# Optimization experiments

Measured on AMD Instinct MI355X. Metric: run time of the kernel, lower is better.

## Reference

```python
import jax, jax.numpy as jnp
import numpy as np

N = 16384          # input points
F = 128            # feature dim (x is (N, 3+F))
POOL = 4           # pooling_factor
M = N // POOL      # number of FPS query points
K = 16             # num_neighbors


def setup_inputs() -> dict:
    key = jax.random.key(0)
    x = jax.random.normal(key, (N, 3 + F), dtype=jnp.float32)
    return {"x": x}


def _fps(coords, m):
    """Furthest point sampling: coords (N,3) -> m indices. Deterministic start at 0."""
    n = coords.shape[0]

    def step(carry, _):
        min_d2, last = carry
        d2 = jnp.sum((coords - coords[last]) ** 2, axis=-1)  # (N,)
        min_d2 = jnp.minimum(min_d2, d2)
        nxt = jnp.argmax(min_d2).astype(jnp.int32)
        return (min_d2, nxt), nxt

    init = (jnp.full((n,), jnp.inf, dtype=coords.dtype), jnp.int32(0))
    _, idxs = jax.lax.scan(step, init, None, length=m - 1)
    return jnp.concatenate([jnp.zeros((1,), dtype=jnp.int32), idxs])


def reference(x):
    coords = x[:, :3]                          # (N,3)
    fps_idx = _fps(coords, M)                  # (M,)
    q_points = coords[fps_idx]                 # (M,3)

    # knn neighbor query: squared distances (M,N), take K nearest
    d2 = jnp.sum((q_points[:, None, :] - coords[None, :, :]) ** 2, axis=-1)
    _, nbr_idx = jax.lax.top_k(-d2, K)         # (M,K)

    s_feats = x[nbr_idx, 3:]                   # (M,K,F) gather
    pooled = jnp.max(s_feats, axis=1)          # feat_mapping='max' -> (M,F)
    return jnp.concatenate([q_points, pooled], axis=-1)  # (M, 3+F)
```

## Files before the change

kernel.cpp:

```cpp
#include <hip/hip_runtime.h>

#define N_PTS 16384
#define ROWF  131
#define M_OUT 4096
#define KNN   16
#define FPS_T 1024

typedef unsigned long long u64;
typedef float f32x2 __attribute__((ext_vector_type(2)));

template <int CTRL, int ROW_MASK>
__device__ __forceinline__ u64 kmax_dpp(u64 k) {
  const int lo = (int)(unsigned)k, hi = (int)(unsigned)(k >> 32);
  const int nlo = __builtin_amdgcn_update_dpp(lo, lo, CTRL, ROW_MASK, 0xf, false);
  const int nhi = __builtin_amdgcn_update_dpp(hi, hi, CTRL, ROW_MASK, 0xf, false);
  const u64 nk = ((u64)(unsigned)nhi << 32) | (unsigned)nlo;
  return nk > k ? nk : k;
}

__global__ void prep_kernel(const float* __restrict__ x,
                            float4* __restrict__ coords4) {
  const int p = blockIdx.x * blockDim.x + threadIdx.x;
  if (p < N_PTS) {
    coords4[p] = make_float4(x[p * ROWF + 0], x[p * ROWF + 1],
                             x[p * ROWF + 2], 0.0f);
  }
}

#define REP16R(F) F(15) F(14) F(13) F(12) F(11) F(10) F(9) F(8) \
                  F(7) F(6) F(5) F(4) F(3) F(2) F(1) F(0)
#define REPP(F) F(0,0,1) F(1,2,3) F(2,4,5) F(3,6,7) \
                F(4,8,9) F(5,10,11) F(6,12,13) F(7,14,15)

__global__
__attribute__((amdgpu_flat_work_group_size(FPS_T, FPS_T)))
__attribute__((amdgpu_waves_per_eu(4, 4)))
void fps_kernel(const float4* __restrict__ coords4, float* __restrict__ out) {
#pragma clang fp contract(off)
  __shared__ u64 s_wkey[2][16];
  const int tid = threadIdx.x, lane = tid & 63, wid = tid >> 6;

#define FPS_DECL(t,a,b) f32x2 PX##t, PY##t, PZ##t; float md##a, md##b;
  REPP(FPS_DECL)
#undef FPS_DECL

#define FPS_INIT(t,a,b) {                                                  \
    const float4 va = coords4[(a << 10) + tid];                            \
    const float4 vb = coords4[(b << 10) + tid];                            \
    PX##t = (f32x2){va.x, vb.x};                                           \
    PY##t = (f32x2){va.y, vb.y};                                           \
    PZ##t = (f32x2){va.z, vb.z};                                           \
    md##a = __int_as_float(0x7f800000);                                    \
    md##b = __int_as_float(0x7f800000); }
  REPP(FPS_INIT)
#undef FPS_INIT

  const float4 q0 = coords4[0];
  float qx = q0.x, qy = q0.y, qz = q0.z;
  if (tid == 0) { out[0] = qx; out[1] = qy; out[2] = qz; }

  for (int s = 1; s < M_OUT; ++s) {
    const f32x2 QX = {qx, qx}, QY = {qy, qy}, QZ = {qz, qz};

#define FPS_UPD(t,a,b) {                                                   \
    const f32x2 dx = PX##t - QX;                                           \
    const f32x2 dy = PY##t - QY;                                           \
    const f32x2 dz = PZ##t - QZ;                                           \
    const f32x2 xx = dx * dx;                                              \
    const f32x2 yy = dy * dy;                                              \
    const f32x2 zz = dz * dz;                                              \
    const f32x2 ss = xx + yy;                                              \
    const f32x2 d2 = ss + zz;                                              \
    md##a = fminf(md##a, d2.x);                                            \
    md##b = fminf(md##b, d2.y); }
    REPP(FPS_UPD)
#undef FPS_UPD

    const float a0 = fmaxf(fmaxf(md0,  md1),  md2);
    const float a1 = fmaxf(fmaxf(md3,  md4),  md5);
    const float a2 = fmaxf(fmaxf(md6,  md7),  md8);
    const float a3 = fmaxf(fmaxf(md9,  md10), md11);
    const float a4 = fmaxf(fmaxf(md12, md13), md14);
    const float b0 = fmaxf(fmaxf(a0, a1), a2);
    const float b1 = fmaxf(fmaxf(a3, a4), md15);
    const float m  = fmaxf(b0, b1);

    unsigned c = 0;
#define FPS_SCAN(j) c = (md##j == m) ? (unsigned)j : c;
    REP16R(FPS_SCAN)
#undef FPS_SCAN
    const unsigned ni = (unsigned)tid + (c << 10);
    u64 k = ((u64)__float_as_uint(m) << 32) | (unsigned)(N_PTS - 1 - ni);

    k = kmax_dpp<0xB1,  0xf>(k);
    k = kmax_dpp<0x4E,  0xf>(k);
    k = kmax_dpp<0x141, 0xf>(k);
    k = kmax_dpp<0x140, 0xf>(k);
    k = kmax_dpp<0x142, 0xa>(k);
    k = kmax_dpp<0x143, 0xc>(k);

    const int par = s & 1;
    if (lane == 63) s_wkey[par][wid] = k;
    __syncthreads();
    u64 kk = s_wkey[par][lane & 15];
    kk = kmax_dpp<0xB1,  0xf>(kk);
    kk = kmax_dpp<0x4E,  0xf>(kk);
    kk = kmax_dpp<0x141, 0xf>(kk);
    kk = kmax_dpp<0x140, 0xf>(kk);

    const int oidx = (N_PTS - 1) - (int)(unsigned)(kk & 0xFFFFFFFFu);
    const float4 wpt = coords4[oidx];
    qx = wpt.x; qy = wpt.y; qz = wpt.z;
    if (tid == 0) {
      float* orow = out + (size_t)s * ROWF;
      orow[0] = qx; orow[1] = qy; orow[2] = qz;
    }
  }
}

__global__ __launch_bounds__(256)
void knn_pool_kernel(const float* __restrict__ x,
                     const float4* __restrict__ coords4,
                     float* __restrict__ out) {
  const int lane = threadIdx.x & 63;
  const int q = blockIdx.x * 4 + (threadIdx.x >> 6);

  const float qx = out[(size_t)q * ROWF + 0];
  const float qy = out[(size_t)q * ROWF + 1];
  const float qz = out[(size_t)q * ROWF + 2];

  u64 h[KNN];
#pragma unroll
  for (int k = 0; k < KNN; ++k) h[k] = ~0ULL;

  for (int c = lane; c < N_PTS; c += 64) {
    const float4 v = coords4[c];
    const float dx = v.x - qx, dy = v.y - qy, dz = v.z - qz;
    const float d2 = __fadd_rn(__fadd_rn(__fmul_rn(dx, dx), __fmul_rn(dy, dy)),
                               __fmul_rn(dz, dz));
    const u64 e = ((u64)__float_as_uint(d2) << 32) | (unsigned)c;
    if (e < h[KNN - 1]) {
#pragma unroll
      for (int k = KNN - 1; k >= 1; --k) {
        const u64 prev = h[k - 1];
        h[k] = (e < prev) ? prev : ((e < h[k]) ? e : h[k]);
      }
      h[0] = (e < h[0]) ? e : h[0];
    }
  }

  int nbr[KNN];
#pragma unroll
  for (int rr = 0; rr < KNN; ++rr) {
    u64 best = h[0];
#pragma unroll
    for (int off = 32; off; off >>= 1) {
      const u64 o = __shfl_xor(best, off);
      best = (o < best) ? o : best;
    }
    nbr[rr] = (int)(unsigned)(best & 0xffffffffULL);
    if (h[0] == best) {
#pragma unroll
      for (int k = 0; k < KNN - 1; ++k) h[k] = h[k + 1];
      h[KNN - 1] = ~0ULL;
    }
  }

  float a0 = __int_as_float(0xff800000), a1 = a0;
#pragma unroll
  for (int rr = 0; rr < KNN; ++rr) {
    const float* row = x + (size_t)nbr[rr] * ROWF + 3;
    a0 = fmaxf(a0, row[lane]);
    a1 = fmaxf(a1, row[lane + 64]);
  }
  float* orow = out + (size_t)q * ROWF + 3;
  orow[lane] = a0;
  orow[lane + 64] = a1;
}

extern "C" void kernel_launch(void* const* d_in, const int* in_sizes, int n_in,
                              void* d_out, int out_size, void* d_ws, size_t ws_size,
                              hipStream_t stream) {
  const float* x = (const float*)d_in[0];
  float* out = (float*)d_out;

  float4* coords4 = (float4*)d_ws;

  hipLaunchKernelGGL(prep_kernel, dim3(64), dim3(256), 0, stream, x, coords4);
  hipLaunchKernelGGL(fps_kernel, dim3(1), dim3(FPS_T), 0, stream, coords4, out);
  hipLaunchKernelGGL(knn_pool_kernel, dim3(M_OUT / 4), dim3(256), 0, stream,
                     x, coords4, out);
}
```

Baseline: 6.649 ms.

## Split FPS argmax into float max reduction then winner-only index min

Each FPS step used one 64-bit (distance, index) key reduction across the block. That is replaced by a 32-bit float max reduction over DPP and shared memory, followed by a second pass. In that pass only the waves holding the global max find their local index and reduce it with an unsigned min. The aim is to cut the per-step cost of the 64-bit DPP moves and compares on the serial FPS critical path. In exchange it adds a second block barrier per iteration plus extra readlane and shared-memory traffic, which may lengthen the serial loop.

```diff
diff --git a/kernel.cpp b/kernel.cpp
--- a/kernel.cpp
+++ b/kernel.cpp
@@ -10,12 +10,16 @@
 typedef float f32x2 __attribute__((ext_vector_type(2)));
 
 template <int CTRL, int ROW_MASK>
-__device__ __forceinline__ u64 kmax_dpp(u64 k) {
-  const int lo = (int)(unsigned)k, hi = (int)(unsigned)(k >> 32);
-  const int nlo = __builtin_amdgcn_update_dpp(lo, lo, CTRL, ROW_MASK, 0xf, false);
-  const int nhi = __builtin_amdgcn_update_dpp(hi, hi, CTRL, ROW_MASK, 0xf, false);
-  const u64 nk = ((u64)(unsigned)nhi << 32) | (unsigned)nlo;
-  return nk > k ? nk : k;
+__device__ __forceinline__ float fmax_dpp(float v) {
+  const int p = __builtin_amdgcn_update_dpp(__float_as_int(v), __float_as_int(v),
+                                            CTRL, ROW_MASK, 0xf, false);
+  return fmaxf(v, __int_as_float(p));
+}
+template <int CTRL, int ROW_MASK>
+__device__ __forceinline__ unsigned umin_dpp(unsigned v) {
+  const unsigned p = (unsigned)__builtin_amdgcn_update_dpp((int)v, (int)v,
+                                            CTRL, ROW_MASK, 0xf, false);
+  return v < p ? v : p;
 }
 
 __global__ void prep_kernel(const float* __restrict__ x,
@@ -37,7 +41,8 @@
 __attribute__((amdgpu_waves_per_eu(4, 4)))
 void fps_kernel(const float4* __restrict__ coords4, float* __restrict__ out) {
 #pragma clang fp contract(off)
-  __shared__ u64 s_wkey[2][16];
+  __shared__ float    s_wmax[2][16];
+  __shared__ unsigned s_arg[2][16];
   const int tid = threadIdx.x, lane = tid & 63, wid = tid >> 6;
 
 #define FPS_DECL(t,a,b) f32x2 PX##t, PY##t, PZ##t; float md##a, md##b;
@@ -55,11 +60,14 @@
   REPP(FPS_INIT)
 #undef FPS_INIT
 
+  if (lane == 63) { s_arg[0][wid] = 0xFFFFFFFFu; s_arg[1][wid] = 0xFFFFFFFFu; }
+
   const float4 q0 = coords4[0];
   float qx = q0.x, qy = q0.y, qz = q0.z;
   if (tid == 0) { out[0] = qx; out[1] = qy; out[2] = qz; }
 
   for (int s = 1; s < M_OUT; ++s) {
+    const int par = s & 1;
     const f32x2 QX = {qx, qx}, QY = {qy, qy}, QZ = {qz, qz};
 
 #define FPS_UPD(t,a,b) {                                                   \
@@ -85,30 +93,51 @@
     const float b1 = fmaxf(fmaxf(a3, a4), md15);
     const float m  = fmaxf(b0, b1);
 
-    unsigned c = 0;
-#define FPS_SCAN(j) c = (md##j == m) ? (unsigned)j : c;
-    REP16R(FPS_SCAN)
+    float fm = m;
+    fm = fmax_dpp<0xB1,  0xf>(fm);
+    fm = fmax_dpp<0x4E,  0xf>(fm);
+    fm = fmax_dpp<0x141, 0xf>(fm);
+    fm = fmax_dpp<0x140, 0xf>(fm);
+    fm = fmax_dpp<0x142, 0xa>(fm);
+    fm = fmax_dpp<0x143, 0xc>(fm);
+
+    if (lane == 63) s_wmax[par][wid] = fm;
+    __syncthreads();
+
+    if (lane == 63) s_arg[par ^ 1][wid] = 0xFFFFFFFFu;
+
+    float bm = s_wmax[par][lane & 15];
+    bm = fmax_dpp<0xB1,  0xf>(bm);
+    bm = fmax_dpp<0x4E,  0xf>(bm);
+    bm = fmax_dpp<0x141, 0xf>(bm);
+    bm = fmax_dpp<0x140, 0xf>(bm);
+
+    const int mwb = __builtin_amdgcn_readlane(__float_as_int(fm), 63);
+    const int mmb = __builtin_amdgcn_readfirstlane(__float_as_int(bm));
+    if (mwb == mmb) {
+      const float mmv = __int_as_float(mmb);
+      unsigned c = 0xFFFFu;
+#define FPS_SCAN(j) c = (md##j == mmv) ? (unsigned)j : c;
+      REP16R(FPS_SCAN)
 #undef FPS_SCAN
-    const unsigned ni = (unsigned)tid + (c << 10);
-    u64 k = ((u64)__float_as_uint(m) << 32) | (unsigned)(N_PTS - 1 - ni);
-
-    k = kmax_dpp<0xB1,  0xf>(k);
-    k = kmax_dpp<0x4E,  0xf>(k);
-    k = kmax_dpp<0x141, 0xf>(k);
-    k = kmax_dpp<0x140, 0xf>(k);
-    k = kmax_dpp<0x142, 0xa>(k);
-    k = kmax_dpp<0x143, 0xc>(k);
-
-    const int par = s & 1;
-    if (lane == 63) s_wkey[par][wid] = k;
+      unsigned nic = (unsigned)tid + (c << 10);
+      nic = umin_dpp<0xB1,  0xf>(nic);
+      nic = umin_dpp<0x4E,  0xf>(nic);
+      nic = umin_dpp<0x141, 0xf>(nic);
+      nic = umin_dpp<0x140, 0xf>(nic);
+      nic = umin_dpp<0x142, 0xa>(nic);
+      nic = umin_dpp<0x143, 0xc>(nic);
+      if (lane == 63) s_arg[par][wid] = nic;
+    }
     __syncthreads();
-    u64 kk = s_wkey[par][lane & 15];
-    kk = kmax_dpp<0xB1,  0xf>(kk);
-    kk = kmax_dpp<0x4E,  0xf>(kk);
-    kk = kmax_dpp<0x141, 0xf>(kk);
-    kk = kmax_dpp<0x140, 0xf>(kk);
-
-    const int oidx = (N_PTS - 1) - (int)(unsigned)(kk & 0xFFFFFFFFu);
+
+    unsigned av = s_arg[par][lane & 15];
+    av = umin_dpp<0xB1,  0xf>(av);
+    av = umin_dpp<0x4E,  0xf>(av);
+    av = umin_dpp<0x141, 0xf>(av);
+    av = umin_dpp<0x140, 0xf>(av);
+
+    const int oidx = (int)av;
     const float4 wpt = coords4[oidx];
     qx = wpt.x; qy = wpt.y; qz = wpt.z;
     if (tid == 0) {
```

Measured after the change: 6.218 ms. 6.5% less time.
